# Kernel optimization log

Measured on AMD Instinct MI355X. Metric: run time of the kernel, lower is better.

The kernel has to match this reference:

```python
import jax, jax.numpy as jnp
import numpy as np

B, S, D = 4, 2048, 1024
H = 16
HD = D // H

def setup_inputs() -> dict:
    key = jax.random.key(0)
    ks = jax.random.split(key, 5)
    x = jax.random.normal(ks[0], (B, S, D), dtype=jnp.float32)
    # PyTorch Linear: y = x @ W.T + b; store W in torch layout [out, in]
    w_qkv = jax.random.normal(ks[1], (3 * D, D), dtype=jnp.float32) * (1.0 / np.sqrt(D))
    b_qkv = jax.random.normal(ks[2], (3 * D,), dtype=jnp.float32) * 0.01
    w_out = jax.random.normal(ks[3], (D, D), dtype=jnp.float32) * (1.0 / np.sqrt(D))
    b_out = jax.random.normal(ks[4], (D,), dtype=jnp.float32) * 0.01
    return {"x": x, "w_qkv": w_qkv, "b_qkv": b_qkv, "w_out": w_out, "b_out": b_out}

def reference(x, w_qkv, b_qkv, w_out, b_out):
    b, s, d = x.shape
    qkv = x @ w_qkv.T + b_qkv                      # [B,S,3D]
    q, k, v = jnp.split(qkv, 3, axis=2)
    # [B,S,D] -> [B,H,S,HD]
    q = q.reshape(b, s, H, HD).transpose(0, 2, 1, 3)
    k = k.reshape(b, s, H, HD).transpose(0, 2, 1, 3)
    v = v.reshape(b, s, H, HD).transpose(0, 2, 1, 3)
    att = jnp.einsum('bhqd,bhkd->bhqk', q, k) / np.sqrt(HD)
    causal = jnp.tril(jnp.ones((s, s), dtype=bool))
    att = jnp.where(causal[None, None], att, -jnp.inf)
    att = jax.nn.softmax(att, axis=-1)
    y = jnp.einsum('bhqk,bhkd->bhqd', att, v)      # [B,H,S,HD]
    y = y.transpose(0, 2, 1, 3).reshape(b, s, d)
    return y @ w_out.T + b_out
```

## Files before the change

### kernel.cpp

```cpp
#include <hip/hip_runtime.h>
#include <hip/hip_bf16.h>

#define DEV __device__ __forceinline__

typedef __attribute__((ext_vector_type(8))) short bf16x8;
typedef __attribute__((ext_vector_type(4))) float f32x4;

#define BB 4
#define SS 2048
#define DD 1024
#define HH 16
#define HDD 64
#define MM (BB * SS)
#define NQT (SS / 128)

DEV short f2bf(float f) {
  unsigned u = __builtin_bit_cast(unsigned, f);
  u = u + 0x7fffu + ((u >> 16) & 1u);
  return (short)(u >> 16);
}

DEV float fexp2(float x) {
  float r;
  asm("v_exp_f32 %0, %1" : "=v"(r) : "v"(x));
  return r;
}
DEV float frcp(float x) {
  float r;
  asm("v_rcp_f32 %0, %1" : "=v"(r) : "v"(x));
  return r;
}
DEV unsigned cvtpk(float a, float b) {
  unsigned r;
  asm("v_cvt_pk_bf16_f32 %0, %1, %2" : "=v"(r) : "v"(a), "v"(b));
  return r;
}

DEV void gload_lds16(const void* g, void* l) {
  __builtin_amdgcn_global_load_lds((const __attribute__((address_space(1))) void*)g,
                                   (__attribute__((address_space(3))) void*)l, 16, 0, 0);
}

DEV int2 xcd_swizzle() {
  const int nx = gridDim.x;
  const int nwg = nx * gridDim.y;
  const int o = blockIdx.y * nx + blockIdx.x;
  const int wid = (o & 7) * (nwg >> 3) + (o >> 3);
  int2 r; r.x = wid % nx; r.y = wid / nx;
  return r;
}

DEV void cast_range(const float* __restrict__ in, unsigned long long* __restrict__ out,
                    int n4, int start, int stride) {
  for (int i = start; i < n4; i += stride) {
    const float4 f = ((const float4*)in)[i];
    unsigned long long a = (unsigned long long)(unsigned short)f2bf(f.x)
        | ((unsigned long long)(unsigned short)f2bf(f.y) << 16)
        | ((unsigned long long)(unsigned short)f2bf(f.z) << 32)
        | ((unsigned long long)(unsigned short)f2bf(f.w) << 48);
    out[i] = a;
  }
}

__global__ __launch_bounds__(256)
void cast3_f32_bf16(const float* __restrict__ x, unsigned long long* __restrict__ ox, int nx4,
                    const float* __restrict__ wq, unsigned long long* __restrict__ owq, int nwq4,
                    const float* __restrict__ wo, unsigned long long* __restrict__ owo, int nwo4) {
  const int start = blockIdx.x * 256 + threadIdx.x;
  const int stride = gridDim.x * 256;
  cast_range(x, ox, nx4, start, stride);
  cast_range(wq, owq, nwq4, start, stride);
  cast_range(wo, owo, nwo4, start, stride);
}

template<int EPI, int BN>
__global__ __launch_bounds__(512, 2)
void gemm_pipe(const short* __restrict__ A, const short* __restrict__ Bw,
               const float* __restrict__ bias,
               short* __restrict__ qo, short* __restrict__ ko, short* __restrict__ vo,
               float* __restrict__ co,
               int M, int N, int K) {
  constexpr int WTN = BN / 4;
  constexpr int FM = 8;
  constexpr int FN = WTN / 16;
  constexpr int NBI = BN / 64;
  __shared__ short sA[2][256 * 64];
  __shared__ short sB[2][BN * 64];
  const int tid = threadIdx.x;
  const int lane = tid & 63;
  const int wid = tid >> 6;
  const int wm = wid >> 2, wn = wid & 3;
  const int2 sw = xcd_swizzle();
  const int m0 = sw.y * 256;
  const int n0 = sw.x * BN;
  const int lr = lane & 15;
  const int lg = lane >> 4;
  const int lm = lr & 7;

  int arow[4], asoff[4], adoff[4];
#pragma unroll
  for (int i = 0; i < 4; ++i) {
    const int e = i * 512 + tid;
    const int row = e >> 3;
    arow[i] = row; asoff[i] = ((e & 7) ^ (row & 7)) * 8; adoff[i] = e * 8;
  }
  int brow[NBI], bsoff[NBI], bdoff[NBI];
#pragma unroll
  for (int i = 0; i < NBI; ++i) {
    const int e = i * 512 + tid;
    const int row = e >> 3;
    brow[i] = row; bsoff[i] = ((e & 7) ^ (row & 7)) * 8; bdoff[i] = e * 8;
  }

  f32x4 acc[FM][FN] = {};
  const int nkt = K >> 6;

#pragma unroll
  for (int i = 0; i < 4; ++i)
    gload_lds16(A + (size_t)(m0 + arow[i]) * K + asoff[i], &sA[0][adoff[i]]);
#pragma unroll
  for (int i = 0; i < NBI; ++i)
    gload_lds16(Bw + (size_t)(n0 + brow[i]) * K + bsoff[i], &sB[0][bdoff[i]]);
#pragma unroll
  for (int i = 0; i < 4; ++i)
    gload_lds16(A + (size_t)(m0 + arow[i]) * K + 64 + asoff[i], &sA[1][adoff[i]]);
#pragma unroll
  for (int i = 0; i < NBI; ++i)
    gload_lds16(Bw + (size_t)(n0 + brow[i]) * K + 64 + bsoff[i], &sB[1][bdoff[i]]);

  for (int kt = 0; kt < nkt; ++kt) {
    const int cur = kt & 1;
    if (kt + 1 < nkt) {
      if constexpr (NBI == 3) asm volatile("s_waitcnt vmcnt(7)" ::: "memory");
      else                    asm volatile("s_waitcnt vmcnt(6)" ::: "memory");
    } else {
      asm volatile("s_waitcnt vmcnt(0)" ::: "memory");
    }
    __builtin_amdgcn_s_barrier();

    bf16x8 afr[FM][2], bfr[FN][2];
#pragma unroll
    for (int ks = 0; ks < 2; ++ks) {
      const int slot = (((ks << 2) + lg) ^ lm) * 8;
#pragma unroll
      for (int i = 0; i < FM; ++i)
        afr[i][ks] = *(const bf16x8*)&sA[cur][(wm * 128 + i * 16 + lr) * 64 + slot];
#pragma unroll
      for (int j = 0; j < FN; ++j)
        bfr[j][ks] = *(const bf16x8*)&sB[cur][(wn * WTN + j * 16 + lr) * 64 + slot];
    }
    asm volatile("s_waitcnt lgkmcnt(0)" ::: "memory");
    __builtin_amdgcn_sched_barrier(0);
    __builtin_amdgcn_s_barrier();

    if (kt + 2 < nkt) {
      const int k2 = (kt + 2) << 6;
#pragma unroll
      for (int i = 0; i < 4; ++i)
        gload_lds16(A + (size_t)(m0 + arow[i]) * K + k2 + asoff[i], &sA[cur][adoff[i]]);
#pragma unroll
      for (int i = 0; i < NBI; ++i)
        gload_lds16(Bw + (size_t)(n0 + brow[i]) * K + k2 + bsoff[i], &sB[cur][bdoff[i]]);
    }

    __builtin_amdgcn_s_setprio(1);
#pragma unroll
    for (int ks = 0; ks < 2; ++ks)
#pragma unroll
      for (int i = 0; i < FM; ++i)
#pragma unroll
        for (int j = 0; j < FN; ++j)
          acc[i][j] = __builtin_amdgcn_mfma_f32_16x16x32_bf16(afr[i][ks], bfr[j][ks], acc[i][j], 0, 0, 0);
    __builtin_amdgcn_s_setprio(0);
  }

#pragma unroll
  for (int i = 0; i < FM; ++i) {
#pragma unroll
    for (int j = 0; j < FN; ++j) {
#pragma unroll
      for (int r = 0; r < 4; ++r) {
        const int row = m0 + wm * 128 + i * 16 + lg * 4 + r;
        const int col = n0 + wn * WTN + j * 16 + lr;
        float v = acc[i][j][r] + bias[col];
        if (EPI == 0) {
          const int part = col >> 10, oo = col & 1023;
          const int h = oo >> 6, d = oo & 63;
          const int bb = row >> 11, s = row & 2047;
          if (part == 0)
            qo[(((size_t)bb * HH + h) * SS + s) * HDD + d] = f2bf(v * 0.18033688f);
          else if (part == 1)
            ko[(((size_t)bb * HH + h) * SS + s) * HDD + d] = f2bf(v);
          else {
            const int q2 = (s >> 2) & 15;
            const int tau = (q2 & 8) | ((q2 & 3) << 1) | ((q2 >> 2) & 1);
            vo[(((size_t)bb * HH + h) * HDD + d) * SS + (s & ~63) + (tau << 2) + (s & 3)] = f2bf(v);
          }
        } else {
          co[(size_t)row * N + col] = v;
        }
      }
    }
  }
}

__global__ __launch_bounds__(256)
void attn_fwd(const short* __restrict__ Q, const short* __restrict__ K,
              const short* __restrict__ V, short* __restrict__ Y) {
  __shared__ short sK[2][64 * 64];
  __shared__ short sV[2][64 * 64];
  const int2 sw = xcd_swizzle();
  const int bh = sw.y;
  const int bx = sw.x;
  const int tid = threadIdx.x, lane = tid & 63, w = tid >> 6;
  const size_t bqk = (size_t)bh * (SS * HDD);
  const size_t bv  = (size_t)bh * (HDD * SS);
  const int b = bh >> 4, h = bh & 15;
  const int lr = lane & 15;
  const int lg = lane >> 4;
  const int lm = lr & 7;

  const int e0 = w * 64 + lane;
  const int e1 = 256 + e0;
  const int r0 = e0 >> 3, s0 = ((e0 & 7) ^ (r0 & 7)) * 8;
  const int r1 = e1 >> 3, s1 = ((e1 & 7) ^ (r1 & 7)) * 8;

  for (int qsel = 0; qsel < 2; ++qsel) {
    const int qt = qsel ? (NQT - 1 - bx) : bx;
    const int q0 = qt * 128;
    const int nkv = 2 * qt + 2;

    __syncthreads();

    {
      const short* gK = K + bqk;
      const short* gV = V + bv;
      gload_lds16(gK + (size_t)r0 * HDD + s0, &sK[0][e0 * 8]);
      gload_lds16(gV + (size_t)r0 * SS + s0, &sV[0][e0 * 8]);
      gload_lds16(gK + (size_t)r1 * HDD + s1, &sK[0][e1 * 8]);
      gload_lds16(gV + (size_t)r1 * SS + s1, &sV[0][e1 * 8]);
    }

    const int qbase = q0 + w * 32;
    bf16x8 qf[2][2];
#pragma unroll
    for (int g = 0; g < 2; ++g)
#pragma unroll
      for (int ks = 0; ks < 2; ++ks)
        qf[g][ks] = *(const bf16x8*)&Q[bqk + (size_t)(qbase + g * 16 + lr) * HDD + ks * 32 + lg * 8];

    f32x4 accO[2][4] = {};
    float m_[2] = {-1e30f, -1e30f}, l_[2] = {0.f, 0.f};

    int cur = 0;
    for (int kt = 0; kt < nkv; ++kt) {
      const int kc0 = kt * 64;
      __syncthreads();
      if (kt < nkv - 1) {
        const short* gK = K + bqk + (size_t)(kc0 + 64) * 64;
        const short* gV = V + bv + kc0 + 64;
        gload_lds16(gK + (size_t)r0 * HDD + s0, &sK[cur ^ 1][e0 * 8]);
        gload_lds16(gV + (size_t)r0 * SS + s0, &sV[cur ^ 1][e0 * 8]);
        gload_lds16(gK + (size_t)r1 * HDD + s1, &sK[cur ^ 1][e1 * 8]);
        gload_lds16(gV + (size_t)r1 * SS + s1, &sV[cur ^ 1][e1 * 8]);
      }

      f32x4 st[2][4] = {};
#pragma unroll
      for (int ks = 0; ks < 2; ++ks) {
#pragma unroll
        for (int nf = 0; nf < 4; ++nf) {
          const int row = nf * 16 + lr;
          const bf16x8 kf = *(const bf16x8*)&sK[cur][row * 64 + (((ks << 2) + lg) ^ lm) * 8];
          st[0][nf] = __builtin_amdgcn_mfma_f32_16x16x32_bf16(kf, qf[0][ks], st[0][nf], 0, 0, 0);
          st[1][nf] = __builtin_amdgcn_mfma_f32_16x16x32_bf16(kf, qf[1][ks], st[1][nf], 0, 0, 0);
        }
      }
      if (kt >= nkv - 2) {
#pragma unroll
        for (int g = 0; g < 2; ++g) {
          const int q = qbase + g * 16 + lr;
#pragma unroll
          for (int nf = 0; nf < 4; ++nf)
#pragma unroll
            for (int r = 0; r < 4; ++r) {
              const int k = kc0 + nf * 16 + lg * 4 + r;
              if (k > q) st[g][nf][r] = -1e30f;
            }
        }
      }

      unsigned u[2][4][2];
#pragma unroll
      for (int g = 0; g < 2; ++g) {
        float rm = -1e30f;
#pragma unroll
        for (int r = 0; r < 4; ++r)
          rm = fmaxf(rm, fmaxf(fmaxf(st[g][0][r], st[g][1][r]), fmaxf(st[g][2][r], st[g][3][r])));
        rm = fmaxf(rm, __shfl_xor(rm, 16));
        rm = fmaxf(rm, __shfl_xor(rm, 32));

        const bool need = rm > m_[g] + 11.5416f;
        if (__any(need)) {
          const float mn = fmaxf(m_[g], rm);
          const float scale = fexp2(m_[g] - mn);
          m_[g] = mn;
          l_[g] *= scale;
#pragma unroll
          for (int r = 0; r < 4; ++r) {
            const float scl = __shfl(scale, (lane & 48) + (lg << 2) + r);
#pragma unroll
            for (int df = 0; df < 4; ++df) accO[g][df][r] *= scl;
          }
        }

        float rs = 0.f;
#pragma unroll
        for (int nf = 0; nf < 4; ++nf)
#pragma unroll
          for (int r = 0; r < 4; ++r) {
            const float p = fexp2(st[g][nf][r] - m_[g]);
            st[g][nf][r] = p;
            rs += p;
          }
        rs += __shfl_xor(rs, 16);
        rs += __shfl_xor(rs, 32);
        l_[g] += rs;

#pragma unroll
        for (int nf = 0; nf < 4; ++nf) {
          u[g][nf][0] = cvtpk(st[g][nf][0], st[g][nf][1]);
          u[g][nf][1] = cvtpk(st[g][nf][2], st[g][nf][3]);
        }
      }

#pragma unroll
      for (int c = 0; c < 2; ++c) {
        int4 pw0, pw1;
        pw0.x = (int)u[0][2 * c][0]; pw0.y = (int)u[0][2 * c][1];
        pw0.z = (int)u[0][2 * c + 1][0]; pw0.w = (int)u[0][2 * c + 1][1];
        pw1.x = (int)u[1][2 * c][0]; pw1.y = (int)u[1][2 * c][1];
        pw1.z = (int)u[1][2 * c + 1][0]; pw1.w = (int)u[1][2 * c + 1][1];
        const bf16x8 pf0 = __builtin_bit_cast(bf16x8, pw0);
        const bf16x8 pf1 = __builtin_bit_cast(bf16x8, pw1);
        const int slot = (((c << 2) + lg) ^ lm) * 8;
#pragma unroll
        for (int df = 0; df < 4; ++df) {
          const bf16x8 vf = *(const bf16x8*)&sV[cur][(df * 16 + lr) * 64 + slot];
          accO[0][df] = __builtin_amdgcn_mfma_f32_16x16x32_bf16(pf0, vf, accO[0][df], 0, 0, 0);
          accO[1][df] = __builtin_amdgcn_mfma_f32_16x16x32_bf16(pf1, vf, accO[1][df], 0, 0, 0);
        }
      }
      cur ^= 1;
    }

#pragma unroll
    for (int g = 0; g < 2; ++g)
#pragma unroll
      for (int r = 0; r < 4; ++r) {
        const float lv = __shfl(l_[g], (lane & 48) + (lg << 2) + r);
        const float inv = frcp(lv);
        const int srow2 = qbase + g * 16 + lg * 4 + r;
#pragma unroll
        for (int df = 0; df < 4; ++df) {
          const int dcol = h * HDD + df * 16 + lr;
          Y[((size_t)b * SS + srow2) * DD + dcol] = f2bf(accO[g][df][r] * inv);
        }
      }
  }
}

extern "C" void kernel_launch(void* const* d_in, const int* in_sizes, int n_in,
                              void* d_out, int out_size, void* d_ws, size_t ws_size,
                              hipStream_t stream) {
  const float* x     = (const float*)d_in[0];
  const float* w_qkv = (const float*)d_in[1];
  const float* b_qkv = (const float*)d_in[2];
  const float* w_out = (const float*)d_in[3];
  const float* b_out = (const float*)d_in[4];
  float* out = (float*)d_out;

  const size_t nx = (size_t)MM * DD;
  const size_t nwq = (size_t)3 * DD * DD;
  const size_t nwo = (size_t)DD * DD;

  short* x_bf    = (short*)d_ws;
  short* wqkv_bf = x_bf + nx;
  short* wout_bf = wqkv_bf + nwq;
  short* q_ws    = wout_bf + nwo;
  short* k_ws    = q_ws + nx;
  short* v_ws    = k_ws + nx;
  short* y_ws    = v_ws + nx;

  cast3_f32_bf16<<<dim3(2048), dim3(256), 0, stream>>>(
      x, (unsigned long long*)x_bf, (int)(nx / 4),
      w_qkv, (unsigned long long*)wqkv_bf, (int)(nwq / 4),
      w_out, (unsigned long long*)wout_bf, (int)(nwo / 4));

  gemm_pipe<0, 192><<<dim3(3 * DD / 192, MM / 256), dim3(512), 0, stream>>>(
      x_bf, wqkv_bf, b_qkv, q_ws, k_ws, v_ws, nullptr, MM, 3 * DD, DD);

  attn_fwd<<<dim3(NQT / 2, BB * HH), dim3(256), 0, stream>>>(q_ws, k_ws, v_ws, y_ws);

  gemm_pipe<1, 128><<<dim3(DD / 128, MM / 256), dim3(512), 0, stream>>>(
      y_ws, wout_bf, b_out, nullptr, nullptr, nullptr, out, MM, DD, DD);
}
```

Baseline: 195.6 us.

## Rewrite GEMM as 4-buffer K=32 pipeline with retuned tile shapes

Replaces the double-buffered K=64 GEMM with a four-buffer pipeline over K=32 slices that prefetches three tiles ahead and uses a single barrier per iteration. The kernel is templated on block and warp tiling; the QKV projection now uses 256x256 tiles and the output projection 128x128 tiles with 256 threads. The aim is to hide more global-load latency and cut synchronisation. The XOR swizzle on shared-memory rows is removed, which may add LDS bank conflicts, and the 256x256 tile raises register pressure.

After: 227.9 us. 16.5% more time.

```diff
diff --git a/kernel.cpp b/kernel.cpp
--- a/kernel.cpp
+++ b/kernel.cpp
@@ -73,104 +73,91 @@
   cast_range(wo, owo, nwo4, start, stride);
 }
 
-template<int EPI, int BN>
-__global__ __launch_bounds__(512, 2)
-void gemm_pipe(const short* __restrict__ A, const short* __restrict__ Bw,
-               const float* __restrict__ bias,
-               short* __restrict__ qo, short* __restrict__ ko, short* __restrict__ vo,
-               float* __restrict__ co,
-               int M, int N, int K) {
-  constexpr int WTN = BN / 4;
-  constexpr int FM = 8;
-  constexpr int FN = WTN / 16;
-  constexpr int NBI = BN / 64;
-  __shared__ short sA[2][256 * 64];
-  __shared__ short sB[2][BN * 64];
+template<int EPI, int BM, int BN, int WN, int THREADS>
+__global__ __launch_bounds__(THREADS, 2)
+void gemm_p4(const short* __restrict__ A, const short* __restrict__ Bw,
+             const float* __restrict__ bias,
+             short* __restrict__ qo, short* __restrict__ ko, short* __restrict__ vo,
+             float* __restrict__ co,
+             int M, int N, int K) {
+  constexpr int NW = THREADS / 64;
+  constexpr int WM = NW / WN;
+  constexpr int WTM = BM / WM, WTN = BN / WN;
+  constexpr int FM = WTM / 16, FN = WTN / 16;
+  constexpr int NA = (4 * BM) / THREADS;
+  constexpr int NB = (4 * BN) / THREADS;
+  __shared__ short sA[4][BM * 32];
+  __shared__ short sB[4][BN * 32];
   const int tid = threadIdx.x;
   const int lane = tid & 63;
   const int wid = tid >> 6;
-  const int wm = wid >> 2, wn = wid & 3;
+  const int wm = wid / WN, wn = wid % WN;
   const int2 sw = xcd_swizzle();
-  const int m0 = sw.y * 256;
-  const int n0 = sw.x * BN;
-  const int lr = lane & 15;
-  const int lg = lane >> 4;
-  const int lm = lr & 7;
-
-  int arow[4], asoff[4], adoff[4];
-#pragma unroll
-  for (int i = 0; i < 4; ++i) {
-    const int e = i * 512 + tid;
-    const int row = e >> 3;
-    arow[i] = row; asoff[i] = ((e & 7) ^ (row & 7)) * 8; adoff[i] = e * 8;
-  }
-  int brow[NBI], bsoff[NBI], bdoff[NBI];
-#pragma unroll
-  for (int i = 0; i < NBI; ++i) {
-    const int e = i * 512 + tid;
-    const int row = e >> 3;
-    brow[i] = row; bsoff[i] = ((e & 7) ^ (row & 7)) * 8; bdoff[i] = e * 8;
+  const int m0 = sw.y * BM, n0 = sw.x * BN;
+  const int lr = lane & 15, lg = lane >> 4;
+
+  int aro[NA], aco[NA], ado[NA];
+#pragma unroll
+  for (int i = 0; i < NA; ++i) {
+    const int c = i * THREADS + tid;
+    aro[i] = c >> 2; aco[i] = (c & 3) * 8; ado[i] = c * 8;
+  }
+  int bro[NB], bco[NB], bdo_[NB];
+#pragma unroll
+  for (int i = 0; i < NB; ++i) {
+    const int c = i * THREADS + tid;
+    bro[i] = c >> 2; bco[i] = (c & 3) * 8; bdo_[i] = c * 8;
+  }
+
+  const int nkt = K >> 5;
+
+#pragma unroll
+  for (int p = 0; p < 3; ++p) {
+    const int kk = p << 5;
+#pragma unroll
+    for (int i = 0; i < NA; ++i)
+      gload_lds16(A + (size_t)(m0 + aro[i]) * K + kk + aco[i], &sA[p][ado[i]]);
+#pragma unroll
+    for (int i = 0; i < NB; ++i)
+      gload_lds16(Bw + (size_t)(n0 + bro[i]) * K + kk + bco[i], &sB[p][bdo_[i]]);
   }
 
   f32x4 acc[FM][FN] = {};
-  const int nkt = K >> 6;
-
-#pragma unroll
-  for (int i = 0; i < 4; ++i)
-    gload_lds16(A + (size_t)(m0 + arow[i]) * K + asoff[i], &sA[0][adoff[i]]);
-#pragma unroll
-  for (int i = 0; i < NBI; ++i)
-    gload_lds16(Bw + (size_t)(n0 + brow[i]) * K + bsoff[i], &sB[0][bdoff[i]]);
-#pragma unroll
-  for (int i = 0; i < 4; ++i)
-    gload_lds16(A + (size_t)(m0 + arow[i]) * K + 64 + asoff[i], &sA[1][adoff[i]]);
-#pragma unroll
-  for (int i = 0; i < NBI; ++i)
-    gload_lds16(Bw + (size_t)(n0 + brow[i]) * K + 64 + bsoff[i], &sB[1][bdoff[i]]);
-
-  for (int kt = 0; kt < nkt; ++kt) {
-    const int cur = kt & 1;
-    if (kt + 1 < nkt) {
-      if constexpr (NBI == 3) asm volatile("s_waitcnt vmcnt(7)" ::: "memory");
-      else                    asm volatile("s_waitcnt vmcnt(6)" ::: "memory");
-    } else {
-      asm volatile("s_waitcnt vmcnt(0)" ::: "memory");
+  for (int t = 0; t < nkt; ++t) {
+    const int buf = t & 3;
+    if (t + 2 < nkt)      asm volatile("s_waitcnt vmcnt(8)" ::: "memory");
+    else if (t + 1 < nkt) asm volatile("s_waitcnt vmcnt(4)" ::: "memory");
+    else                  asm volatile("s_waitcnt vmcnt(0)" ::: "memory");
+    __builtin_amdgcn_s_barrier();
+    __builtin_amdgcn_sched_barrier(0);
+
+    if (t + 3 < nkt) {
+      const int kk = (t + 3) << 5;
+      const int pb = (t + 3) & 3;
+#pragma unroll
+      for (int i = 0; i < NA; ++i)
+        gload_lds16(A + (size_t)(m0 + aro[i]) * K + kk + aco[i], &sA[pb][ado[i]]);
+#pragma unroll
+      for (int i = 0; i < NB; ++i)
+        gload_lds16(Bw + (size_t)(n0 + bro[i]) * K + kk + bco[i], &sB[pb][bdo_[i]]);
     }
-    __builtin_amdgcn_s_barrier();
-
-    bf16x8 afr[FM][2], bfr[FN][2];
-#pragma unroll
-    for (int ks = 0; ks < 2; ++ks) {
-      const int slot = (((ks << 2) + lg) ^ lm) * 8;
-#pragma unroll
-      for (int i = 0; i < FM; ++i)
-        afr[i][ks] = *(const bf16x8*)&sA[cur][(wm * 128 + i * 16 + lr) * 64 + slot];
-#pragma unroll
-      for (int j = 0; j < FN; ++j)
-        bfr[j][ks] = *(const bf16x8*)&sB[cur][(wn * WTN + j * 16 + lr) * 64 + slot];
-    }
+
+    bf16x8 afr[FM], bfr[FN];
+#pragma unroll
+    for (int i = 0; i < FM; ++i)
+      afr[i] = *(const bf16x8*)&sA[buf][(wm * WTM + i * 16 + lr) * 32 + lg * 8];
+#pragma unroll
+    for (int j = 0; j < FN; ++j)
+      bfr[j] = *(const bf16x8*)&sB[buf][(wn * WTN + j * 16 + lr) * 32 + lg * 8];
     asm volatile("s_waitcnt lgkmcnt(0)" ::: "memory");
     __builtin_amdgcn_sched_barrier(0);
-    __builtin_amdgcn_s_barrier();
-
-    if (kt + 2 < nkt) {
-      const int k2 = (kt + 2) << 6;
-#pragma unroll
-      for (int i = 0; i < 4; ++i)
-        gload_lds16(A + (size_t)(m0 + arow[i]) * K + k2 + asoff[i], &sA[cur][adoff[i]]);
-#pragma unroll
-      for (int i = 0; i < NBI; ++i)
-        gload_lds16(Bw + (size_t)(n0 + brow[i]) * K + k2 + bsoff[i], &sB[cur][bdoff[i]]);
-    }
 
     __builtin_amdgcn_s_setprio(1);
 #pragma unroll
-    for (int ks = 0; ks < 2; ++ks)
-#pragma unroll
-      for (int i = 0; i < FM; ++i)
-#pragma unroll
-        for (int j = 0; j < FN; ++j)
-          acc[i][j] = __builtin_amdgcn_mfma_f32_16x16x32_bf16(afr[i][ks], bfr[j][ks], acc[i][j], 0, 0, 0);
+    for (int i = 0; i < FM; ++i)
+#pragma unroll
+      for (int j = 0; j < FN; ++j)
+        acc[i][j] = __builtin_amdgcn_mfma_f32_16x16x32_bf16(afr[i], bfr[j], acc[i][j], 0, 0, 0);
     __builtin_amdgcn_s_setprio(0);
   }
 
@@ -180,7 +167,7 @@
     for (int j = 0; j < FN; ++j) {
 #pragma unroll
       for (int r = 0; r < 4; ++r) {
-        const int row = m0 + wm * 128 + i * 16 + lg * 4 + r;
+        const int row = m0 + wm * WTM + i * 16 + lg * 4 + r;
         const int col = n0 + wn * WTN + j * 16 + lr;
         float v = acc[i][j][r] + bias[col];
         if (EPI == 0) {
@@ -397,11 +384,11 @@
       w_qkv, (unsigned long long*)wqkv_bf, (int)(nwq / 4),
       w_out, (unsigned long long*)wout_bf, (int)(nwo / 4));
 
-  gemm_pipe<0, 192><<<dim3(3 * DD / 192, MM / 256), dim3(512), 0, stream>>>(
+  gemm_p4<0, 256, 256, 4, 512><<<dim3(3 * DD / 256, MM / 256), dim3(512), 0, stream>>>(
       x_bf, wqkv_bf, b_qkv, q_ws, k_ws, v_ws, nullptr, MM, 3 * DD, DD);
 
   attn_fwd<<<dim3(NQT / 2, BB * HH), dim3(256), 0, stream>>>(q_ws, k_ws, v_ws, y_ws);
 
-  gemm_pipe<1, 128><<<dim3(DD / 128, MM / 256), dim3(512), 0, stream>>>(
+  gemm_p4<1, 128, 128, 2, 256><<<dim3(DD / 128, MM / 128), dim3(256), 0, stream>>>(
       y_ws, wout_bf, b_out, nullptr, nullptr, nullptr, out, MM, DD, DD);
 }
```
